# Kernel tuning notes

Hardware: AMD Instinct MI355X
Metric: run time of the kernel (lower is better)

## Reference

```python
import jax, jax.numpy as jnp
import numpy as np


def setup_inputs() -> dict:
    key = jax.random.key(0)
    k1, k2 = jax.random.split(key)
    x = jax.random.normal(k1, (4, 2048, 2048), dtype=jnp.float32)
    weight = jax.random.normal(k2, (8192, 2048), dtype=jnp.float32) * 0.02
    return {"x": x, "weight": weight, "bits": 8}


def reference(x, weight, bits):
    # ---- activation quantization (per-row int8-style) ----
    scale = jnp.clip(jnp.max(jnp.abs(x), axis=-1, keepdims=True), 1e-5)  # [..., 1]
    max_val = (1 << (bits - 1)) - 1  # 127 for 8 bits
    x_q = jnp.clip(jnp.round(x * (max_val / scale)), -max_val, max_val)

    # ---- ternary weight quantization (-1, 0, 1) ----
    w_scale = jnp.mean(jnp.abs(weight))
    w_q = jnp.where(weight > 0.5 * w_scale, 1.0, 0.0) + jnp.where(
        weight < -0.5 * w_scale, -1.0, 0.0
    )

    # ---- dequantized linear: (x_q @ (w_q * w_scale)^T) / x_scale ----
    out = jnp.einsum("bsi,oi->bso", x_q, w_q * w_scale) / scale

    # ---- squared ReLU ----
    return jnp.maximum(out, 0.0) ** 2
```

## Files before the change

### kernel.cpp

```cpp
#include <hip/hip_runtime.h>
#include <hip/hip_bf16.h>

typedef __attribute__((ext_vector_type(4))) int i32x4;

#define M_DIM 8192
#define N_DIM 8192
#define K_DIM 2048
#define BK 128
#define WCOUNT (N_DIM * K_DIM)

__global__ __launch_bounds__(256) void k_abs_partial(const float* __restrict__ w,
                                                     float* __restrict__ part) {
    int tid = blockIdx.x * 256 + threadIdx.x;
    const float4* w4 = (const float4*)w;
    float s = 0.0f;
    const int total4 = WCOUNT / 4;
    for (int i = tid; i < total4; i += 2048 * 256) {
        float4 v = w4[i];
        s += fabsf(v.x) + fabsf(v.y) + fabsf(v.z) + fabsf(v.w);
    }
    #pragma unroll
    for (int off = 1; off < 64; off <<= 1) s += __shfl_xor(s, off);
    __shared__ float red[4];
    if ((threadIdx.x & 63) == 0) red[threadIdx.x >> 6] = s;
    __syncthreads();
    if (threadIdx.x == 0)
        part[blockIdx.x] = (red[0] + red[1]) + (red[2] + red[3]);
}

__global__ __launch_bounds__(256) void k_abs_final(const float* __restrict__ part,
                                                   float* __restrict__ sum) {
    int t = threadIdx.x;
    float s = 0.0f;
    #pragma unroll
    for (int i = 0; i < 8; i++) s += part[t + i * 256];
    #pragma unroll
    for (int off = 1; off < 64; off <<= 1) s += __shfl_xor(s, off);
    __shared__ float red[4];
    if ((t & 63) == 0) red[t >> 6] = s;
    __syncthreads();
    if (t == 0) sum[0] = (red[0] + red[1]) + (red[2] + red[3]);
}

__global__ __launch_bounds__(256) void k_wquant(const float* __restrict__ w,
                                                const float* __restrict__ sum,
                                                unsigned int* __restrict__ wq) {
    const float thr = 0.5f * (sum[0] * (1.0f / 16777216.0f));
    int tid = blockIdx.x * 256 + threadIdx.x;
    const float4* w4 = (const float4*)w;
    const int total4 = WCOUNT / 4;
    for (int i = tid; i < total4; i += 2048 * 256) {
        float4 v = w4[i];
        union { signed char c[4]; unsigned int u; } q;
        q.c[0] = v.x > thr ? 1 : (v.x < -thr ? -1 : 0);
        q.c[1] = v.y > thr ? 1 : (v.y < -thr ? -1 : 0);
        q.c[2] = v.z > thr ? 1 : (v.z < -thr ? -1 : 0);
        q.c[3] = v.w > thr ? 1 : (v.w < -thr ? -1 : 0);
        wq[i] = q.u;
    }
}

__global__ __launch_bounds__(256) void k_xquant(const float* __restrict__ x,
                                                signed char* __restrict__ xq,
                                                float* __restrict__ scale) {
    const int row = blockIdx.x;
    const int t = threadIdx.x;
    const float4* xr = (const float4*)(x + (size_t)row * K_DIM);
    float4 a = xr[t * 2];
    float4 b = xr[t * 2 + 1];
    float m = fmaxf(fmaxf(fmaxf(fabsf(a.x), fabsf(a.y)), fmaxf(fabsf(a.z), fabsf(a.w))),
                    fmaxf(fmaxf(fabsf(b.x), fabsf(b.y)), fmaxf(fabsf(b.z), fabsf(b.w))));
    #pragma unroll
    for (int off = 1; off < 64; off <<= 1) m = fmaxf(m, __shfl_xor(m, off));
    __shared__ float red[4];
    if ((t & 63) == 0) red[t >> 6] = m;
    __syncthreads();
    m = fmaxf(fmaxf(red[0], red[1]), fmaxf(red[2], red[3]));
    const float sc = fmaxf(m, 1e-5f);
    if (t == 0) scale[row] = sc;
    const float r = 127.0f / sc;
    float q[8] = {a.x, a.y, a.z, a.w, b.x, b.y, b.z, b.w};
    union { signed char c[8]; uint2 v; } pk;
    #pragma unroll
    for (int j = 0; j < 8; j++) {
        float v = rintf(q[j] * r);
        v = fminf(fmaxf(v, -127.0f), 127.0f);
        pk.c[j] = (signed char)v;
    }
    *(uint2*)(xq + (size_t)row * K_DIM + t * 8) = pk.v;
}

#define GLDS16(g, l)                                                                   \
    __builtin_amdgcn_global_load_lds((const __attribute__((address_space(1))) void*)(g), \
                                     (__attribute__((address_space(3))) void*)(l), 16, 0, 0)

#define AOFF(b, h) ((b) * 32768 + (h) * 16384)
#define BOFF(b, h) (65536 + (b) * 32768 + (h) * 16384)
#define BAR __builtin_amdgcn_s_barrier()
#define VMCNT4 do { asm volatile("s_waitcnt vmcnt(4)" ::: "memory"); __builtin_amdgcn_sched_barrier(0); } while (0)
#define VMCNT0 do { asm volatile("s_waitcnt vmcnt(0)" ::: "memory"); __builtin_amdgcn_sched_barrier(0); } while (0)

__global__ __launch_bounds__(512, 2) void k_gemm(const signed char* __restrict__ Aq,
                                                 const signed char* __restrict__ Bq,
                                                 const float* __restrict__ scale,
                                                 const float* __restrict__ sum,
                                                 float* __restrict__ out) {
    __shared__ signed char lds[131072];

    const int t = threadIdx.x;
    const int lane = t & 63;
    const int wid = t >> 6;
    const int wm = wid >> 2;
    const int wn = wid & 3;
    const int lane4 = lane & 15;
    const int hi = lane >> 4;

    const int bid = blockIdx.x;
    const int swzb = ((bid & 7) << 7) | (bid >> 3);
    const int brow = swzb >> 5;
    const int bcol = swzb & 31;

    const int r0 = t >> 3;
    const int r1 = 64 + r0;
    const int g0 = ((t & 7) ^ ((t >> 4) & 7)) << 4;
    const int g1 = (((t + 512) & 7) ^ (((t + 512) >> 4) & 7)) << 4;
    const int sa0 = r0 * K_DIM + g0;
    const int sa1 = r1 * K_DIM + g1;
    const int dst0 = wid * 1024;
    const int dst1 = wid * 1024 + 8192;

    const signed char* Abase = Aq + (size_t)(brow * 256) * K_DIM;
    const signed char* Bbase = Bq + (size_t)(bcol * 256) * K_DIM;

#define STG(gb, ldsoff, half, kt) do {                                                  \
        GLDS16((gb) + (half) * (128 * K_DIM) + (kt) * BK + sa0, lds + (ldsoff) + dst0); \
        GLDS16((gb) + (half) * (128 * K_DIM) + (kt) * BK + sa1, lds + (ldsoff) + dst1); \
    } while (0)

    const int swz0 = (hi ^ (lane4 >> 1)) << 4;
    const int swz1 = ((4 + hi) ^ (lane4 >> 1)) << 4;
    const int aB0 = AOFF(0, wm) + lane4 * 128;
    const int aB1 = AOFF(1, wm) + lane4 * 128;
    const int bB0 = BOFF(0, wn >> 1) + ((wn & 1) * 64 + lane4) * 128;
    const int bB1 = BOFF(1, wn >> 1) + ((wn & 1) * 64 + lane4) * 128;

    i32x4 acc[8][4];
    #pragma unroll
    for (int m = 0; m < 8; m++)
        #pragma unroll
        for (int n = 0; n < 4; n++) acc[m][n] = (i32x4){0, 0, 0, 0};
    i32x4 fa0[8], fa1[8], fb0[4], fb1[4];

#define RDA(base, mlo) do { _Pragma("unroll") for (int m_ = 0; m_ < 4; m_++) {          \
        fa0[(mlo) + m_] = *(const i32x4*)&lds[(base) + ((mlo) + m_) * 2048 + swz0];     \
        fa1[(mlo) + m_] = *(const i32x4*)&lds[(base) + ((mlo) + m_) * 2048 + swz1]; } } while (0)
#define RDB(base, nlo) do { _Pragma("unroll") for (int n_ = 0; n_ < 2; n_++) {          \
        fb0[(nlo) + n_] = *(const i32x4*)&lds[(base) + ((nlo) + n_) * 2048 + swz0];     \
        fb1[(nlo) + n_] = *(const i32x4*)&lds[(base) + ((nlo) + n_) * 2048 + swz1]; } } while (0)
#define MM(mlo, nlo) do { __builtin_amdgcn_s_setprio(1);                                \
        _Pragma("unroll") for (int m_ = 0; m_ < 4; m_++)                                \
        _Pragma("unroll") for (int n_ = 0; n_ < 2; n_++) {                              \
            acc[(mlo) + m_][(nlo) + n_] = __builtin_amdgcn_mfma_i32_16x16x64_i8(        \
                fa0[(mlo) + m_], fb0[(nlo) + n_], acc[(mlo) + m_][(nlo) + n_], 0, 0, 0);\
            acc[(mlo) + m_][(nlo) + n_] = __builtin_amdgcn_mfma_i32_16x16x64_i8(        \
                fa1[(mlo) + m_], fb1[(nlo) + n_], acc[(mlo) + m_][(nlo) + n_], 0, 0, 0);\
        } __builtin_amdgcn_s_setprio(0); } while (0)

    STG(Abase, AOFF(0, 0), 0, 0); STG(Abase, AOFF(0, 1), 1, 0);
    STG(Bbase, BOFF(0, 0), 0, 0); STG(Bbase, BOFF(0, 1), 1, 0);
    STG(Abase, AOFF(1, 0), 0, 1); STG(Abase, AOFF(1, 1), 1, 1);
    STG(Bbase, BOFF(1, 0), 0, 1); STG(Bbase, BOFF(1, 1), 1, 1);
    asm volatile("s_waitcnt vmcnt(8)" ::: "memory");
    __builtin_amdgcn_sched_barrier(0);
    BAR;

    #pragma unroll 1
    for (int i = 0; i < 8; i++) {
        const int kt = 2 * i;
        if (i >= 1) { STG(Bbase, BOFF(1, 0), 0, kt + 1); STG(Bbase, BOFF(1, 1), 1, kt + 1); }
        RDA(aB0, 0); RDB(bB0, 0);
        MM(0, 0);
        BAR;
        RDA(aB0, 4); RDB(bB0, 2);
        MM(0, 2);
        BAR;
        MM(4, 0);
        BAR;
        if (i <= 6) { STG(Abase, AOFF(0, 0), 0, kt + 2); STG(Abase, AOFF(0, 1), 1, kt + 2); }
        MM(4, 2);
        if (i <= 6) VMCNT4; else VMCNT0;
        BAR;
        if (i <= 6) { STG(Bbase, BOFF(0, 0), 0, kt + 2); STG(Bbase, BOFF(0, 1), 1, kt + 2); }
        RDA(aB1, 0); RDB(bB1, 0);
        MM(0, 0);
        BAR;
        RDA(aB1, 4); RDB(bB1, 2);
        MM(0, 2);
        BAR;
        MM(4, 0);
        BAR;
        if (i <= 6) { STG(Abase, AOFF(1, 0), 0, kt + 3); STG(Abase, AOFF(1, 1), 1, kt + 3); }
        MM(4, 2);
        if (i <= 6) VMCNT4; else VMCNT0;
        BAR;
    }

    const float wsc = sum[0] * (1.0f / 16777216.0f);
    const int rb = brow * 256 + wm * 128 + hi * 4;
    const int cb = bcol * 256 + wn * 64 + lane4;
    #pragma unroll
    for (int m = 0; m < 8; m++) {
        #pragma unroll
        for (int j = 0; j < 4; j++) {
            const int grow = rb + m * 16 + j;
            const float coef = wsc / scale[grow];
            #pragma unroll
            for (int n = 0; n < 4; n++) {
                float v = (float)acc[m][n][j] * coef;
                v = fmaxf(v, 0.0f);
                out[(size_t)grow * N_DIM + cb + n * 16] = v * v;
            }
        }
    }
#undef STG
#undef RDA
#undef RDB
#undef MM
}

extern "C" void kernel_launch(void* const* d_in, const int* in_sizes, int n_in,
                              void* d_out, int out_size, void* d_ws, size_t ws_size,
                              hipStream_t stream) {
    const float* x = (const float*)d_in[0];
    const float* w = (const float*)d_in[1];
    float* out = (float*)d_out;

    char* ws = (char*)d_ws;
    float* sum   = (float*)ws;
    float* part  = (float*)(ws + 256);
    float* scale = (float*)(ws + 16384);
    signed char* xq = (signed char*)(ws + 65536);
    signed char* wq = (signed char*)(ws + 65536 + 16777216);

    k_abs_partial<<<2048, 256, 0, stream>>>(w, part);
    k_abs_final<<<1, 256, 0, stream>>>(part, sum);
    k_wquant<<<2048, 256, 0, stream>>>(w, sum, (unsigned int*)wq);
    k_xquant<<<M_DIM, 256, 0, stream>>>(x, xq, scale);
    k_gemm<<<dim3(1024), 512, 0, stream>>>(xq, wq, scale, sum, out);
}
```

Before: 202.0 us.

## Interleave global-to-LDS staging across MFMA phases and remap blocks into 4x4 tiles

```diff
diff --git a/kernel.cpp b/kernel.cpp
--- a/kernel.cpp
+++ b/kernel.cpp
@@ -97,7 +97,9 @@
 #define AOFF(b, h) ((b) * 32768 + (h) * 16384)
 #define BOFF(b, h) (65536 + (b) * 32768 + (h) * 16384)
 #define BAR __builtin_amdgcn_s_barrier()
-#define VMCNT4 do { asm volatile("s_waitcnt vmcnt(4)" ::: "memory"); __builtin_amdgcn_sched_barrier(0); } while (0)
+#define LGKM8 do { asm volatile("s_waitcnt lgkmcnt(8)" ::: "memory"); __builtin_amdgcn_sched_barrier(0); } while (0)
+#define LGKM0 do { asm volatile("s_waitcnt lgkmcnt(0)" ::: "memory"); __builtin_amdgcn_sched_barrier(0); } while (0)
+#define VMCNT2 do { asm volatile("s_waitcnt vmcnt(2)" ::: "memory"); __builtin_amdgcn_sched_barrier(0); } while (0)
 #define VMCNT0 do { asm volatile("s_waitcnt vmcnt(0)" ::: "memory"); __builtin_amdgcn_sched_barrier(0); } while (0)
 
 __global__ __launch_bounds__(512, 2) void k_gemm(const signed char* __restrict__ Aq,
@@ -116,16 +118,18 @@
     const int hi = lane >> 4;
 
     const int bid = blockIdx.x;
-    const int swzb = ((bid & 7) << 7) | (bid >> 3);
-    const int brow = swzb >> 5;
-    const int bcol = swzb & 31;
+    const int xcd = bid & 7;
+    const int s_ = bid >> 3;
+    const int scol = s_ >> 4;
+    const int w_ = s_ & 15;
+    const int brow = xcd * 4 + (w_ >> 2);
+    const int bcol = scol * 4 + (w_ & 3);
 
     const int r0 = t >> 3;
-    const int r1 = 64 + r0;
     const int g0 = ((t & 7) ^ ((t >> 4) & 7)) << 4;
     const int g1 = (((t + 512) & 7) ^ (((t + 512) >> 4) & 7)) << 4;
     const int sa0 = r0 * K_DIM + g0;
-    const int sa1 = r1 * K_DIM + g1;
+    const int sa1 = (64 + r0) * K_DIM + g1;
     const int dst0 = wid * 1024;
     const int dst1 = wid * 1024 + 8192;
 
@@ -151,10 +155,10 @@
         for (int n = 0; n < 4; n++) acc[m][n] = (i32x4){0, 0, 0, 0};
     i32x4 fa0[8], fa1[8], fb0[4], fb1[4];
 
-#define RDA(base, mlo) do { _Pragma("unroll") for (int m_ = 0; m_ < 4; m_++) {          \
+#define RDA4(mlo, base) do { _Pragma("unroll") for (int m_ = 0; m_ < 4; m_++) {         \
         fa0[(mlo) + m_] = *(const i32x4*)&lds[(base) + ((mlo) + m_) * 2048 + swz0];     \
         fa1[(mlo) + m_] = *(const i32x4*)&lds[(base) + ((mlo) + m_) * 2048 + swz1]; } } while (0)
-#define RDB(base, nlo) do { _Pragma("unroll") for (int n_ = 0; n_ < 2; n_++) {          \
+#define RDB2(nlo, base) do { _Pragma("unroll") for (int n_ = 0; n_ < 2; n_++) {         \
         fb0[(nlo) + n_] = *(const i32x4*)&lds[(base) + ((nlo) + n_) * 2048 + swz0];     \
         fb1[(nlo) + n_] = *(const i32x4*)&lds[(base) + ((nlo) + n_) * 2048 + swz1]; } } while (0)
 #define MM(mlo, nlo) do { __builtin_amdgcn_s_setprio(1);                                \
@@ -166,42 +170,56 @@
                 fa1[(mlo) + m_], fb1[(nlo) + n_], acc[(mlo) + m_][(nlo) + n_], 0, 0, 0);\
         } __builtin_amdgcn_s_setprio(0); } while (0)
 
-    STG(Abase, AOFF(0, 0), 0, 0); STG(Abase, AOFF(0, 1), 1, 0);
-    STG(Bbase, BOFF(0, 0), 0, 0); STG(Bbase, BOFF(0, 1), 1, 0);
-    STG(Abase, AOFF(1, 0), 0, 1); STG(Abase, AOFF(1, 1), 1, 1);
-    STG(Bbase, BOFF(1, 0), 0, 1); STG(Bbase, BOFF(1, 1), 1, 1);
-    asm volatile("s_waitcnt vmcnt(8)" ::: "memory");
-    __builtin_amdgcn_sched_barrier(0);
+    STG(Bbase, BOFF(0, 0), 0, 0);
+    STG(Bbase, BOFF(0, 1), 1, 0);
+    STG(Abase, AOFF(0, 0), 0, 0);
+    STG(Abase, AOFF(0, 1), 1, 0);
+    STG(Bbase, BOFF(1, 0), 0, 1);
+    VMCNT2;
     BAR;
 
     #pragma unroll 1
     for (int i = 0; i < 8; i++) {
         const int kt = 2 * i;
-        if (i >= 1) { STG(Bbase, BOFF(1, 0), 0, kt + 1); STG(Bbase, BOFF(1, 1), 1, kt + 1); }
-        RDA(aB0, 0); RDB(bB0, 0);
+        STG(Bbase, BOFF(1, 1), 1, kt + 1);
+        RDA4(0, aB0); RDB2(0, bB0);
+        LGKM8;
+        BAR; LGKM0;
         MM(0, 0);
         BAR;
-        RDA(aB0, 4); RDB(bB0, 2);
+        STG(Abase, AOFF(1, 0), 0, kt + 1);
+        RDB2(2, bB0);
+        BAR; LGKM0;
         MM(0, 2);
         BAR;
+        STG(Abase, AOFF(1, 1), 1, kt + 1);
+        RDA4(4, aB0);
+        BAR; LGKM0;
         MM(4, 0);
         BAR;
-        if (i <= 6) { STG(Abase, AOFF(0, 0), 0, kt + 2); STG(Abase, AOFF(0, 1), 1, kt + 2); }
+        if (i < 7) STG(Bbase, BOFF(0, 0), 0, kt + 2);
         MM(4, 2);
-        if (i <= 6) VMCNT4; else VMCNT0;
-        BAR;
-        if (i <= 6) { STG(Bbase, BOFF(0, 0), 0, kt + 2); STG(Bbase, BOFF(0, 1), 1, kt + 2); }
-        RDA(aB1, 0); RDB(bB1, 0);
+        if (i < 7) VMCNT2; else VMCNT0;
+        BAR;
+        if (i < 7) STG(Bbase, BOFF(0, 1), 1, kt + 2);
+        RDA4(0, aB1); RDB2(0, bB1);
+        LGKM8;
+        BAR; LGKM0;
         MM(0, 0);
         BAR;
-        RDA(aB1, 4); RDB(bB1, 2);
+        if (i < 7) STG(Abase, AOFF(0, 0), 0, kt + 2);
+        RDB2(2, bB1);
+        BAR; LGKM0;
         MM(0, 2);
         BAR;
+        if (i < 7) STG(Abase, AOFF(0, 1), 1, kt + 2);
+        RDA4(4, aB1);
+        BAR; LGKM0;
         MM(4, 0);
         BAR;
-        if (i <= 6) { STG(Abase, AOFF(1, 0), 0, kt + 3); STG(Abase, AOFF(1, 1), 1, kt + 3); }
+        if (i < 7) STG(Bbase, BOFF(1, 0), 0, kt + 3);
         MM(4, 2);
-        if (i <= 6) VMCNT4; else VMCNT0;
+        if (i < 7) VMCNT2;
         BAR;
     }
 
@@ -223,8 +241,8 @@
         }
     }
 #undef STG
-#undef RDA
-#undef RDB
+#undef RDA4
+#undef RDB2
 #undef MM
 }
 
```

Measured after the change: 205.1 us. Within noise of the previous version (+1.5%).
